# Kernel optimization log

Hardware: AMD Instinct MI355X
Metric: run time of the kernel (lower is better)

The kernel has to match this reference:

```python
import jax, jax.numpy as jnp
import numpy as np

H = 128  # hidden width


def _mlp(xy, W0, b0, W1, b1, W2, b2, W3, b3):
    # xy: [..., 2] -> [..., 1], tanh MLP
    h = jnp.tanh(xy @ W0 + b0)
    h = jnp.tanh(h @ W1 + b1)
    h = jnp.tanh(h @ W2 + b2)
    return h @ W3 + b3


def setup_inputs() -> dict:
    key = jax.random.key(0)
    ks = jax.random.split(key, 8)
    n_int, n_bd = 262144, 16384
    inp = {
        "xy_int": jax.random.uniform(ks[0], (n_int, 2), dtype=jnp.float32),
        "f": jax.random.normal(ks[1], (n_int, 1), dtype=jnp.float32),
        "xy_bd": jax.random.uniform(ks[2], (n_bd, 2), dtype=jnp.float32),
        "g": jax.random.normal(ks[3], (n_bd, 1), dtype=jnp.float32),
        # Glorot-ish scaled weights
        "W0": jax.random.normal(ks[4], (2, H), dtype=jnp.float32) / np.sqrt(2.0),
        "b0": jnp.zeros((H,), jnp.float32),
        "W1": jax.random.normal(ks[5], (H, H), dtype=jnp.float32) / np.sqrt(H),
        "b1": jnp.zeros((H,), jnp.float32),
        "W2": jax.random.normal(ks[6], (H, H), dtype=jnp.float32) / np.sqrt(H),
        "b2": jnp.zeros((H,), jnp.float32),
        "W3": jax.random.normal(ks[7], (H, 1), dtype=jnp.float32) / np.sqrt(H),
        "b3": jnp.zeros((1,), jnp.float32),
    }
    return inp


def reference(xy_int, f, xy_bd, g, W0, b0, W1, b1, W2, b2, W3, b3):
    params = (W0, b0, W1, b1, W2, b2, W3, b3)
    n_int = xy_int.shape[0]
    n_bd = xy_bd.shape[0]

    # boundary loss: 0.5/n_bd * ||u(xy_bd) - g||^2
    pred_bd = _mlp(xy_bd, *params)
    diff_bd = pred_bd.reshape(-1) - g.reshape(-1)
    loss_bound = 0.5 / n_bd * jnp.sum(diff_bd * diff_bd)

    # interior PDE residual: u_xx + u_yy (Laplacian) per collocation point
    def u_scalar(p):  # p: [2] -> scalar
        return _mlp(p[None, :], *params)[0, 0]

    def lap_point(p):
        return jnp.trace(jax.hessian(u_scalar)(p))  # 2x2 Hessian trace

    pred_f = jax.vmap(lap_point)(xy_int)  # [n_int]
    diff_f = pred_f.reshape(-1) - f.reshape(-1)
    loss_f = 0.5 / n_int * jnp.sum(diff_f * diff_f)

    return (loss_bound, loss_f)
```

## Files before the change

### kernel.cpp

```cpp
#include <hip/hip_runtime.h>

#define HID 128
#define PTS 32
#define FRAGS_PER_W 2048
#define WS_ELEMS (FRAGS_PER_W * 8)
#define TANH_K 2.885390081777927f

typedef float v4f  __attribute__((ext_vector_type(4)));
typedef float v16f __attribute__((ext_vector_type(16)));
typedef short s8v  __attribute__((ext_vector_type(8)));

__device__ __forceinline__ unsigned short f2bf(float f) {
    unsigned u = __builtin_bit_cast(unsigned, f);
    u = (u + 0x7FFFu + ((u >> 16) & 1u)) >> 16;
    return (unsigned short)u;
}

#if __has_builtin(__builtin_amdgcn_cvt_pk_bf16_f32)
typedef __bf16 bf16x2 __attribute__((ext_vector_type(2)));
__device__ __forceinline__ unsigned pk2(float f0, float f1) {
    return __builtin_bit_cast(unsigned, __builtin_amdgcn_cvt_pk_bf16_f32(f0, f1));
}
#else
__device__ __forceinline__ unsigned pk2(float f0, float f1) {
    unsigned u0 = __builtin_bit_cast(unsigned, f0);
    unsigned u1 = __builtin_bit_cast(unsigned, f1);
    u0 += 0x7FFFu + ((u0 >> 16) & 1u);
    u1 += 0x7FFFu + ((u1 >> 16) & 1u);
    return __builtin_amdgcn_perm(u1, u0, 0x07060302u);
}
#endif
__device__ __forceinline__ uint2 pk4(const float* f) {
    uint2 h;
    h.x = pk2(f[0], f[1]);
    h.y = pk2(f[2], f[3]);
    return h;
}

__device__ __forceinline__ float tanh_pre(float xp) {
#if __has_builtin(__builtin_amdgcn_exp2f)
    float e = __builtin_amdgcn_exp2f(xp);
#else
    float e = __expf(xp * 0.6931471805599453f);
#endif
    float r = __builtin_amdgcn_rcpf(e + 1.0f);
    return fmaf(-2.0f, r, 1.0f);
}

__device__ __forceinline__ void* sb_at(unsigned short* sBh, int row, int colh) {
    return (char*)sBh + (row << 8) + (((colh << 1)) ^ ((row & 15) << 4));
}

__global__ __launch_bounds__(256) void prep_w_kernel(
    const float* __restrict__ W1, const float* __restrict__ W2,
    const float* __restrict__ b1, const float* __restrict__ b2,
    unsigned short* __restrict__ ws, float* __restrict__ out)
{
    const int t = blockIdx.x * 256 + threadIdx.x;
    if (t < 2) out[t] = 0.0f;
    if (t < 256) {
        float* bK = (float*)(ws + (size_t)2 * WS_ELEMS);
        bK[t] = TANH_K * ((t < 128) ? b1[t] : b2[t - 128]);
    }
    const int w = t >> 11;
    const int r = t & 2047;
    const int mw = r >> 9;
    const int ks8 = (r >> 6) & 7;
    const int lane = r & 63;
    const int m = mw * 32 + (lane & 31);
    const int kb = ks8 * 16 + (lane >> 5) * 8;
    const float* W = w ? W2 : W1;
    s8v hv;
    #pragma unroll
    for (int i = 0; i < 8; ++i)
        hv[i] = (short)f2bf(W[(kb + i) * HID + m]);
    *(s8v*)&ws[((size_t)w * FRAGS_PER_W + r) * 8] = hv;
}

template <int NC>
__device__ __forceinline__ void run_pinn(
    const float* __restrict__ xy, const float* __restrict__ tgt,
    const float* __restrict__ W0, const float* __restrict__ b0,
    const float* __restrict__ bK, const float* __restrict__ W3,
    const float* __restrict__ b3,
    const unsigned short* __restrict__ ws, float* __restrict__ out_slot,
    float scale, int pbase, unsigned short* sBh, float* sPart)
{
    const int tid  = threadIdx.x;
    const int lane = tid & 63;
    const int mw   = tid >> 6;
    const int l31  = lane & 31;
    const int kh   = lane >> 5;

    s8v wf[8];
    #pragma unroll
    for (int q = 0; q < 8; ++q)
        wf[q] = *(const s8v*)&ws[(size_t)(mw * 512 + q * 64 + lane) * 8];

    {
        const int tj = tid & 31, tp = tid >> 5;
        const int j0 = tj * 4, p0 = tp * 4;
        const v4f wxv = *(const v4f*)&W0[j0];
        const v4f wyv = *(const v4f*)&W0[HID + j0];
        const v4f b0v = *(const v4f*)&b0[j0];
        float wx[4], wy[4], m2s2[4], wxK[4], wyK[4], bbK[4];
        #pragma unroll
        for (int jj = 0; jj < 4; ++jj) {
            wx[jj] = wxv[jj];
            wy[jj] = wyv[jj];
            wxK[jj] = TANH_K * wx[jj];
            wyK[jj] = TANH_K * wy[jj];
            bbK[jj] = TANH_K * b0v[jj];
            m2s2[jj] = -2.0f * fmaf(wx[jj], wx[jj], wy[jj] * wy[jj]);
        }
        #pragma unroll
        for (int pp = 0; pp < 4; ++pp) {
            const int p = p0 + pp;
            const float2 t2 = ((const float2*)xy)[pbase + p];
            float chv[NC][4];
            #pragma unroll
            for (int jj = 0; jj < 4; ++jj) {
                float xp = fmaf(t2.x, wxK[jj], fmaf(t2.y, wyK[jj], bbK[jj]));
                float a = tanh_pre(xp);
                chv[0][jj] = a;
                if (NC == 4) {
                    float t = fmaf(-a, a, 1.0f);
                    chv[1][jj] = t * wx[jj];
                    chv[2][jj] = t * wy[jj];
                    chv[3][jj] = (a * t) * m2s2[jj];
                }
            }
            #pragma unroll
            for (int c = 0; c < NC; ++c)
                *(uint2*)sb_at(sBh, c * 32 + p, j0) = pk4(chv[c]);
        }
    }
    __syncthreads();

    v16f acc[NC];

    #pragma unroll
    for (int L = 0; L < 2; ++L) {
        #pragma unroll
        for (int nt = 0; nt < NC; ++nt) acc[nt] = (v16f)0.0f;

        __builtin_amdgcn_s_setprio(1);
        #pragma unroll
        for (int q = 0; q < 8; ++q) {
            const int koff = q * 16 + kh * 8;
            #pragma unroll
            for (int nt = 0; nt < NC; ++nt) {
                s8v bh = *(const s8v*)sb_at(sBh, nt * 32 + l31, koff);
                acc[nt] = __builtin_amdgcn_mfma_f32_32x32x16_bf16(
                    wf[q], bh, acc[nt], 0, 0, 0);
            }
        }
        __builtin_amdgcn_s_setprio(0);

        if (L == 0) {
            __syncthreads();
            #pragma unroll
            for (int q = 0; q < 8; ++q)
                wf[q] = *(const s8v*)&ws[WS_ELEMS + (size_t)(mw * 512 + q * 64 + lane) * 8];
            #pragma unroll
            for (int g = 0; g < 4; ++g) {
                const int j0g = mw * 32 + 8 * g + 4 * kh;
                const v4f bbK = *(const v4f*)&bK[j0g];
                float chv[NC][4];
                #pragma unroll
                for (int r = 0; r < 4; ++r) {
                    float a = tanh_pre(fmaf(acc[0][g * 4 + r], TANH_K, bbK[r]));
                    chv[0][r] = a;
                    if (NC == 4) {
                        float t = fmaf(-a, a, 1.0f);
                        float zx = acc[1][g * 4 + r], zy = acc[2][g * 4 + r],
                              zl = acc[3][g * 4 + r];
                        float s2 = fmaf(zx, zx, zy * zy);
                        float u  = fmaf(-(a + a), s2, zl);
                        chv[1][r] = t * zx;
                        chv[2][r] = t * zy;
                        chv[3][r] = t * u;
                    }
                }
                #pragma unroll
                for (int c = 0; c < NC; ++c)
                    *(uint2*)sb_at(sBh, c * 32 + l31, j0g) = pk4(chv[c]);
            }
            __syncthreads();
        }
    }

    {
        float part = 0.0f;
        #pragma unroll
        for (int g = 0; g < 4; ++g) {
            const int j0g = mw * 32 + 8 * g + 4 * kh;
            const v4f bbK = *(const v4f*)&bK[HID + j0g];
            const v4f w3 = *(const v4f*)&W3[j0g];
            #pragma unroll
            for (int r = 0; r < 4; ++r) {
                float a = tanh_pre(fmaf(acc[0][g * 4 + r], TANH_K, bbK[r]));
                float v;
                if (NC == 1) {
                    v = a;
                } else {
                    float t = fmaf(-a, a, 1.0f);
                    float zx = acc[1][g * 4 + r], zy = acc[2][g * 4 + r],
                          zl = acc[3][g * 4 + r];
                    float s2 = fmaf(zx, zx, zy * zy);
                    v = t * fmaf(-(a + a), s2, zl);
                }
                part = fmaf(v, w3[r], part);
            }
        }
        part += __shfl_xor(part, 32, 64);
        if (kh == 0) sPart[mw * 32 + l31] = part;
        __syncthreads();
        if (mw == 0) {
            const int p = l31;
            float pred = (sPart[p] + sPart[32 + p]) + (sPart[64 + p] + sPart[96 + p])
                       + ((NC == 1) ? b3[0] : 0.0f);
            float d = pred - tgt[pbase + p];
            float sq = (kh == 0) ? d * d : 0.0f;
            sq += __shfl_xor(sq, 1, 64);
            sq += __shfl_xor(sq, 2, 64);
            sq += __shfl_xor(sq, 4, 64);
            sq += __shfl_xor(sq, 8, 64);
            sq += __shfl_xor(sq, 16, 64);
            sq += __shfl_xor(sq, 32, 64);
            if (lane == 0) atomicAdd(out_slot, sq * scale);
        }
    }
}

__global__ __launch_bounds__(256, 4) void pinn_mfma_kernel(
    const float* __restrict__ xy_int, const float* __restrict__ f_t,
    const float* __restrict__ xy_bd, const float* __restrict__ g_t,
    const float* __restrict__ W0, const float* __restrict__ b0,
    const float* __restrict__ bK, const float* __restrict__ W3,
    const float* __restrict__ b3,
    const unsigned short* __restrict__ ws, float* __restrict__ out,
    int gi, float scale_int, float scale_bd)
{
    extern __shared__ char smem_raw[];
    unsigned short* sBh = (unsigned short*)smem_raw;
    float* sPart = (float*)(sBh + 4 * 32 * 128);

    const int b = (int)blockIdx.x;
    if (b >= gi)
        run_pinn<1>(xy_bd, g_t, W0, b0, bK, W3, b3, ws,
                    out + 0, scale_bd, (b - gi) * PTS, sBh, sPart);
    else
        run_pinn<4>(xy_int, f_t, W0, b0, bK, W3, b3, ws,
                    out + 1, scale_int, b * PTS, sBh, sPart);
}

extern "C" void kernel_launch(void* const* d_in, const int* in_sizes, int n_in,
                              void* d_out, int out_size, void* d_ws, size_t ws_size,
                              hipStream_t stream) {
    const float* xy_int = (const float*)d_in[0];
    const float* f      = (const float*)d_in[1];
    const float* xy_bd  = (const float*)d_in[2];
    const float* g      = (const float*)d_in[3];
    const float* W0 = (const float*)d_in[4];
    const float* b0 = (const float*)d_in[5];
    const float* W1 = (const float*)d_in[6];
    const float* b1 = (const float*)d_in[7];
    const float* W2 = (const float*)d_in[8];
    const float* b2 = (const float*)d_in[9];
    const float* W3 = (const float*)d_in[10];
    const float* b3 = (const float*)d_in[11];
    float* out = (float*)d_out;
    unsigned short* ws = (unsigned short*)d_ws;
    const float* bK = (const float*)(ws + (size_t)2 * WS_ELEMS);

    const int n_int = in_sizes[0] / 2;
    const int n_bd  = in_sizes[2] / 2;

    prep_w_kernel<<<16, 256, 0, stream>>>(W1, W2, b1, b2, ws, out);

    const int smem = 4 * 32 * 128 * 2 + 128 * 4;
    const int gi = n_int / PTS;
    const int gb = n_bd / PTS;

    pinn_mfma_kernel<<<gi + gb, 256, smem, stream>>>(
        xy_int, f, xy_bd, g, W0, b0, bK, W3, b3, ws, out,
        gi, 0.5f / (float)n_int, 0.5f / (float)n_bd);
}
```

Before: 194.4 us.

## Drop weight prep kernel; convert W1/W2 to bf16 inline and interleave boundary blocks

```diff
diff --git a/kernel.cpp b/kernel.cpp
--- a/kernel.cpp
+++ b/kernel.cpp
@@ -2,19 +2,11 @@
 
 #define HID 128
 #define PTS 32
-#define FRAGS_PER_W 2048
-#define WS_ELEMS (FRAGS_PER_W * 8)
 #define TANH_K 2.885390081777927f
 
 typedef float v4f  __attribute__((ext_vector_type(4)));
 typedef float v16f __attribute__((ext_vector_type(16)));
 typedef short s8v  __attribute__((ext_vector_type(8)));
-
-__device__ __forceinline__ unsigned short f2bf(float f) {
-    unsigned u = __builtin_bit_cast(unsigned, f);
-    u = (u + 0x7FFFu + ((u >> 16) & 1u)) >> 16;
-    return (unsigned short)u;
-}
 
 #if __has_builtin(__builtin_amdgcn_cvt_pk_bf16_f32)
 typedef __bf16 bf16x2 __attribute__((ext_vector_type(2)));
@@ -51,39 +43,24 @@
     return (char*)sBh + (row << 8) + (((colh << 1)) ^ ((row & 15) << 4));
 }
 
-__global__ __launch_bounds__(256) void prep_w_kernel(
-    const float* __restrict__ W1, const float* __restrict__ W2,
-    const float* __restrict__ b1, const float* __restrict__ b2,
-    unsigned short* __restrict__ ws, float* __restrict__ out)
-{
-    const int t = blockIdx.x * 256 + threadIdx.x;
-    if (t < 2) out[t] = 0.0f;
-    if (t < 256) {
-        float* bK = (float*)(ws + (size_t)2 * WS_ELEMS);
-        bK[t] = TANH_K * ((t < 128) ? b1[t] : b2[t - 128]);
-    }
-    const int w = t >> 11;
-    const int r = t & 2047;
-    const int mw = r >> 9;
-    const int ks8 = (r >> 6) & 7;
-    const int lane = r & 63;
-    const int m = mw * 32 + (lane & 31);
-    const int kb = ks8 * 16 + (lane >> 5) * 8;
-    const float* W = w ? W2 : W1;
-    s8v hv;
+__device__ __forceinline__ s8v conv_frag(const float* __restrict__ W, int kb, int m) {
+    float w[8];
     #pragma unroll
-    for (int i = 0; i < 8; ++i)
-        hv[i] = (short)f2bf(W[(kb + i) * HID + m]);
-    *(s8v*)&ws[((size_t)w * FRAGS_PER_W + r) * 8] = hv;
+    for (int i = 0; i < 8; ++i) w[i] = W[(kb + i) * HID + m];
+    uint4 u;
+    u.x = pk2(w[0], w[1]); u.y = pk2(w[2], w[3]);
+    u.z = pk2(w[4], w[5]); u.w = pk2(w[6], w[7]);
+    return __builtin_bit_cast(s8v, u);
 }
 
 template <int NC>
 __device__ __forceinline__ void run_pinn(
     const float* __restrict__ xy, const float* __restrict__ tgt,
     const float* __restrict__ W0, const float* __restrict__ b0,
-    const float* __restrict__ bK, const float* __restrict__ W3,
-    const float* __restrict__ b3,
-    const unsigned short* __restrict__ ws, float* __restrict__ out_slot,
+    const float* __restrict__ W1, const float* __restrict__ b1,
+    const float* __restrict__ W2, const float* __restrict__ b2,
+    const float* __restrict__ W3, const float* __restrict__ b3,
+    float* __restrict__ out_slot,
     float scale, int pbase, unsigned short* sBh, float* sPart)
 {
     const int tid  = threadIdx.x;
@@ -92,10 +69,12 @@
     const int l31  = lane & 31;
     const int kh   = lane >> 5;
 
+    const int am = mw * 32 + l31;
+
     s8v wf[8];
     #pragma unroll
     for (int q = 0; q < 8; ++q)
-        wf[q] = *(const s8v*)&ws[(size_t)(mw * 512 + q * 64 + lane) * 8];
+        wf[q] = conv_frag(W1, q * 16 + kh * 8, am);
 
     {
         const int tj = tid & 31, tp = tid >> 5;
@@ -144,7 +123,6 @@
         #pragma unroll
         for (int nt = 0; nt < NC; ++nt) acc[nt] = (v16f)0.0f;
 
-        __builtin_amdgcn_s_setprio(1);
         #pragma unroll
         for (int q = 0; q < 8; ++q) {
             const int koff = q * 16 + kh * 8;
@@ -155,17 +133,17 @@
                     wf[q], bh, acc[nt], 0, 0, 0);
             }
         }
-        __builtin_amdgcn_s_setprio(0);
 
         if (L == 0) {
             __syncthreads();
             #pragma unroll
             for (int q = 0; q < 8; ++q)
-                wf[q] = *(const s8v*)&ws[WS_ELEMS + (size_t)(mw * 512 + q * 64 + lane) * 8];
+                wf[q] = conv_frag(W2, q * 16 + kh * 8, am);
             #pragma unroll
             for (int g = 0; g < 4; ++g) {
                 const int j0g = mw * 32 + 8 * g + 4 * kh;
-                const v4f bbK = *(const v4f*)&bK[j0g];
+                const v4f bb1 = *(const v4f*)&b1[j0g];
+                const v4f bbK = TANH_K * bb1;
                 float chv[NC][4];
                 #pragma unroll
                 for (int r = 0; r < 4; ++r) {
@@ -195,7 +173,8 @@
         #pragma unroll
         for (int g = 0; g < 4; ++g) {
             const int j0g = mw * 32 + 8 * g + 4 * kh;
-            const v4f bbK = *(const v4f*)&bK[HID + j0g];
+            const v4f bb2 = *(const v4f*)&b2[j0g];
+            const v4f bbK = TANH_K * bb2;
             const v4f w3 = *(const v4f*)&W3[j0g];
             #pragma unroll
             for (int r = 0; r < 4; ++r) {
@@ -237,22 +216,33 @@
     const float* __restrict__ xy_int, const float* __restrict__ f_t,
     const float* __restrict__ xy_bd, const float* __restrict__ g_t,
     const float* __restrict__ W0, const float* __restrict__ b0,
-    const float* __restrict__ bK, const float* __restrict__ W3,
-    const float* __restrict__ b3,
-    const unsigned short* __restrict__ ws, float* __restrict__ out,
-    int gi, float scale_int, float scale_bd)
+    const float* __restrict__ W1, const float* __restrict__ b1,
+    const float* __restrict__ W2, const float* __restrict__ b2,
+    const float* __restrict__ W3, const float* __restrict__ b3,
+    float* __restrict__ out,
+    int gi, int gb, float scale_int, float scale_bd)
 {
     extern __shared__ char smem_raw[];
     unsigned short* sBh = (unsigned short*)smem_raw;
     float* sPart = (float*)(sBh + 4 * 32 * 128);
 
     const int b = (int)blockIdx.x;
-    if (b >= gi)
-        run_pinn<1>(xy_bd, g_t, W0, b0, bK, W3, b3, ws,
-                    out + 0, scale_bd, (b - gi) * PTS, sBh, sPart);
+    bool is_bd; int idx;
+    if (gi == gb * 16) {
+        const int q = b / 17, r = b - q * 17;
+        is_bd = (r == 16);
+        idx = is_bd ? q : q * 16 + r;
+    } else {
+        is_bd = (b >= gi);
+        idx = is_bd ? b - gi : b;
+    }
+
+    if (is_bd)
+        run_pinn<1>(xy_bd, g_t, W0, b0, W1, b1, W2, b2, W3, b3,
+                    out + 0, scale_bd, idx * PTS, sBh, sPart);
     else
-        run_pinn<4>(xy_int, f_t, W0, b0, bK, W3, b3, ws,
-                    out + 1, scale_int, b * PTS, sBh, sPart);
+        run_pinn<4>(xy_int, f_t, W0, b0, W1, b1, W2, b2, W3, b3,
+                    out + 1, scale_int, idx * PTS, sBh, sPart);
 }
 
 extern "C" void kernel_launch(void* const* d_in, const int* in_sizes, int n_in,
@@ -271,19 +261,17 @@
     const float* W3 = (const float*)d_in[10];
     const float* b3 = (const float*)d_in[11];
     float* out = (float*)d_out;
-    unsigned short* ws = (unsigned short*)d_ws;
-    const float* bK = (const float*)(ws + (size_t)2 * WS_ELEMS);
 
     const int n_int = in_sizes[0] / 2;
     const int n_bd  = in_sizes[2] / 2;
 
-    prep_w_kernel<<<16, 256, 0, stream>>>(W1, W2, b1, b2, ws, out);
+    hipMemsetAsync(out, 0, 2 * sizeof(float), stream);
 
     const int smem = 4 * 32 * 128 * 2 + 128 * 4;
     const int gi = n_int / PTS;
     const int gb = n_bd / PTS;
 
     pinn_mfma_kernel<<<gi + gb, 256, smem, stream>>>(
-        xy_int, f, xy_bd, g, W0, b0, bK, W3, b3, ws, out,
-        gi, 0.5f / (float)n_int, 0.5f / (float)n_bd);
-}
+        xy_int, f, xy_bd, g, W0, b0, W1, b1, W2, b2, W3, b3, out,
+        gi, gb, 0.5f / (float)n_int, 0.5f / (float)n_bd);
+}
```

After: 263.3 us. 35.5% more time.
